# Kernel tuning notes

Measured on AMD Instinct MI355X. Metric: run time of the kernel, lower is better.

The kernel has to match this reference:

```python
import jax, jax.numpy as jnp
import numpy as np

B, T, C, H = 4, 4096, 1024, 64  # batch, seq_len, embedding_dimension, head_size


def setup_inputs() -> dict:
    key = jax.random.key(0)
    kx, kq, kk, kv = jax.random.split(key, 4)
    x = jax.random.normal(kx, (B, T, C), dtype=jnp.float32)
    # nn.Linear(C, H, bias=False) -> weight applied as x @ W with W:[C,H]
    s = 1.0 / np.sqrt(C)
    Wq = jax.random.normal(kq, (C, H), dtype=jnp.float32) * s
    Wk = jax.random.normal(kk, (C, H), dtype=jnp.float32) * s
    Wv = jax.random.normal(kv, (C, H), dtype=jnp.float32) * s
    return {"x": x, "Wq": Wq, "Wk": Wk, "Wv": Wv}


def reference(x, Wq, Wk, Wv):
    Bx, Tx, Cx = x.shape
    q = x @ Wq  # [B,T,H]
    k = x @ Wk  # [B,T,H]
    v = x @ Wv  # [B,T,H]
    # NOTE: original scales by C**-0.5 (embedding dim), not head_size**-0.5
    wei = jnp.einsum('bqh,bkh->bqk', q, k) * (Cx ** -0.5)  # [B,T,T]
    causal = jnp.tril(jnp.ones((Tx, Tx), dtype=bool))
    wei = jnp.where(causal, wei, -jnp.inf)
    wei = jax.nn.softmax(wei, axis=-1)
    out = jnp.einsum('bqk,bkh->bqh', wei, v)  # [B,T,H]
    return out
```

## Files before the change

kernel.cpp:

```cpp
#include <hip/hip_runtime.h>
#include <math.h>

#define BATCH 4
#define SEQ   4096
#define EMB   1024
#define HDIM  64
#define NSPLIT 4

typedef __attribute__((ext_vector_type(8))) short bf16x8;
typedef __attribute__((ext_vector_type(4))) float f32x4;
typedef __attribute__((ext_vector_type(4))) unsigned int u32x4;

#define MFMA16(a, b, c) __builtin_amdgcn_mfma_f32_16x16x32_bf16(a, b, c, 0, 0, 0)

__device__ __forceinline__ unsigned short f2bf(float f) {
  unsigned int u = __float_as_uint(f);
  u = (u + 0x7FFFu + ((u >> 16) & 1u)) >> 16;
  return (unsigned short)u;
}

__device__ __forceinline__ float fexp2(float x) {
  float r;
  asm("v_exp_f32 %0, %1" : "=v"(r) : "v"(x));
  return r;
}

__global__ __launch_bounds__(256) void wt_kernel(
    const float* __restrict__ Wq, const float* __restrict__ Wk,
    const float* __restrict__ Wv, unsigned short* __restrict__ wt) {
  __shared__ float tile[64][65];
  const int bid = blockIdx.x;
  const int m = bid >> 4, kt = bid & 15;
  const float* W = (m == 0) ? Wq : (m == 1) ? Wk : Wv;
  const int tid = threadIdx.x;
  {
    const int r = tid >> 2, c4 = tid & 3;
    const float* src = W + (size_t)(kt * 64 + r) * 64 + c4 * 16;
#pragma unroll
    for (int j = 0; j < 4; ++j) {
      float4 a = *(const float4*)(src + j * 4);
      tile[r][c4 * 16 + j * 4 + 0] = a.x;
      tile[r][c4 * 16 + j * 4 + 1] = a.y;
      tile[r][c4 * 16 + j * 4 + 2] = a.z;
      tile[r][c4 * 16 + j * 4 + 3] = a.w;
    }
  }
  __syncthreads();
  {
    const int col = tid >> 2, kq = tid & 3;
    unsigned short o[16];
#pragma unroll
    for (int j = 0; j < 16; ++j) o[j] = f2bf(tile[kq * 16 + j][col]);
    unsigned short* dst = wt + (size_t)(m * 64 + col) * 1024 + kt * 64 + kq * 16;
    *(bf16x8*)(dst)     = *(bf16x8*)&o[0];
    *(bf16x8*)(dst + 8) = *(bf16x8*)&o[8];
  }
}

__global__ __launch_bounds__(512) void qkv_mfma_kernel(
    const float* __restrict__ x, const unsigned short* __restrict__ wt,
    unsigned short* __restrict__ qb, unsigned short* __restrict__ kb,
    unsigned short* __restrict__ vt) {
  __shared__ __align__(16) unsigned short xs[64 * 64];
  __shared__ __align__(16) unsigned short ws[192 * 64];
  const int tid  = threadIdx.x;
  const int lane = tid & 63, wid = tid >> 6;
  const int g = lane >> 4, p = lane & 15;
  const int mt = wid >> 2, wq = wid & 3;
  const size_t row0 = (size_t)blockIdx.x * 64;

  const int sr = tid >> 3, sc = tid & 7;
  const float* xp = x + (row0 + sr) * EMB + sc * 8;

  f32x4 acc[2][3];
#pragma unroll
  for (int rt = 0; rt < 2; ++rt)
#pragma unroll
    for (int ct = 0; ct < 3; ++ct) acc[rt][ct] = (f32x4){0.f, 0.f, 0.f, 0.f};

  float4 rx[2];
  bf16x8 rw[3];
#pragma unroll
  for (int j = 0; j < 2; ++j) rx[j] = *(const float4*)(xp + j * 4);
#pragma unroll
  for (int it = 0; it < 3; ++it) {
    int i = tid + it * 512, col = i >> 3, cc = i & 7;
    rw[it] = *(const bf16x8*)(wt + (size_t)col * 1024 + cc * 8);
  }

  for (int kc = 0; kc < 16; ++kc) {
    __syncthreads();
#pragma unroll
    for (int j = 0; j < 2; ++j) {
      ushort4 h;
      h.x = f2bf(rx[j].x); h.y = f2bf(rx[j].y);
      h.z = f2bf(rx[j].z); h.w = f2bf(rx[j].w);
      *(ushort4*)((char*)xs + ((sr * 128 + sc * 16 + j * 8) ^ ((sr & 7) << 4))) = h;
    }
#pragma unroll
    for (int it = 0; it < 3; ++it) {
      int i = tid + it * 512, col = i >> 3, cc = i & 7;
      *(bf16x8*)((char*)ws + ((col * 128 + cc * 16) ^ ((col & 7) << 4))) = rw[it];
    }
    if (kc < 15) {
      const float* xpn = xp + (kc + 1) * 64;
#pragma unroll
      for (int j = 0; j < 2; ++j) rx[j] = *(const float4*)(xpn + j * 4);
#pragma unroll
      for (int it = 0; it < 3; ++it) {
        int i = tid + it * 512, col = i >> 3, cc = i & 7;
        rw[it] = *(const bf16x8*)(wt + (size_t)col * 1024 + (kc + 1) * 64 + cc * 8);
      }
    }
    __syncthreads();
#pragma unroll
    for (int ks = 0; ks < 2; ++ks) {
      bf16x8 af[2];
#pragma unroll
      for (int rt = 0; rt < 2; ++rt) {
        int row = mt * 32 + rt * 16 + p;
        af[rt] = *(const bf16x8*)((char*)xs +
                 ((row * 128 + ks * 64 + g * 16) ^ ((row & 7) << 4)));
      }
#pragma unroll
      for (int ct = 0; ct < 3; ++ct) {
        int col = wq * 48 + ct * 16 + p;
        bf16x8 bfr = *(const bf16x8*)((char*)ws +
                     ((col * 128 + ks * 64 + g * 16) ^ ((col & 7) << 4)));
#pragma unroll
        for (int rt = 0; rt < 2; ++rt)
          acc[rt][ct] = MFMA16(af[rt], bfr, acc[rt][ct]);
      }
    }
  }

  const int b     = (int)(row0 >> 12);
  const int tbase = (int)(row0 & 4095);
  unsigned short* vtb = vt + (((size_t)b * 64 + (tbase >> 6)) * 64) * 64;
#pragma unroll
  for (int rt = 0; rt < 2; ++rt)
#pragma unroll
    for (int ct = 0; ct < 3; ++ct) {
      const int c0  = wq * 48 + ct * 16;
      const int mtx = c0 >> 6;
      const int col = (c0 & 63) + p;
#pragma unroll
      for (int r = 0; r < 4; ++r) {
        const int row = mt * 32 + rt * 16 + 4 * g + r;
        const float vf = acc[rt][ct][r];
        if (mtx == 0)      qb[(row0 + row) * HDIM + col] = f2bf(vf * 0.0450843714f);
        else if (mtx == 1) kb[(row0 + row) * HDIM + col] = f2bf(vf);
        else               vtb[(size_t)col * 64 + row]   = f2bf(vf);
      }
    }
}

__device__ __forceinline__ void tile_body_lds(
    const unsigned short* __restrict__ sKb, const unsigned short* __restrict__ sVb,
    int qrel, bool diag,
    const bf16x8& qf0, const bf16x8& qf1,
    int p, int g, int cA0, int cA1, int srcA, int srcB, bool hi,
    float& m, float& l, f32x4 (&o)[4]) {
  f32x4 sc4[4];
#pragma unroll
  for (int t = 0; t < 4; ++t) {
    const int row = 16 * t + p;
    bf16x8 a0 = *(const bf16x8*)((const char*)sKb + row * 128 + cA0);
    bf16x8 a1 = *(const bf16x8*)((const char*)sKb + row * 128 + cA1);
    f32x4 a = (f32x4){0.f, 0.f, 0.f, 0.f};
    a = MFMA16(a0, qf0, a);
    a = MFMA16(a1, qf1, a);
    sc4[t] = a;
  }
  if (diag) {
#pragma unroll
    for (int t = 0; t < 4; ++t)
#pragma unroll
      for (int r = 0; r < 4; ++r)
        if (16 * t + 4 * g + r > qrel) sc4[t][r] = -1e30f;
  }
  float tm = -3e38f;
#pragma unroll
  for (int t = 0; t < 4; ++t)
#pragma unroll
    for (int r = 0; r < 4; ++r) tm = fmaxf(tm, sc4[t][r]);
  tm = fmaxf(tm, __shfl_xor(tm, 16));
  tm = fmaxf(tm, __shfl_xor(tm, 32));
  if (__any(tm > m + 11.5f)) {
    float mn = fmaxf(m, tm);
    float c = fexp2(m - mn);
    l *= c;
#pragma unroll
    for (int mi = 0; mi < 4; ++mi) o[mi] *= c;
    m = mn;
  }
  float psum = 0.f;
#pragma unroll
  for (int t = 0; t < 4; ++t)
#pragma unroll
    for (int r = 0; r < 4; ++r) {
      float pv = fexp2(sc4[t][r] - m);
      sc4[t][r] = pv;
      psum += pv;
    }
  l += psum;
  unsigned int pk[4][2];
#pragma unroll
  for (int t = 0; t < 4; ++t) {
    asm("v_cvt_pk_bf16_f32 %0, %1, %2"
        : "=v"(pk[t][0]) : "v"(sc4[t][0]), "v"(sc4[t][1]));
    asm("v_cvt_pk_bf16_f32 %0, %1, %2"
        : "=v"(pk[t][1]) : "v"(sc4[t][2]), "v"(sc4[t][3]));
  }
  u32x4 wb0, wb1;
#pragma unroll
  for (int h2 = 0; h2 < 2; ++h2) {
    const int src = h2 ? srcB : srcA;
    unsigned c0 = (unsigned)__shfl((int)pk[0][0], src);
    unsigned c1 = (unsigned)__shfl((int)pk[1][0], src);
    wb0[2 * h2 + 0] = hi ? c1 : c0;
    unsigned d0 = (unsigned)__shfl((int)pk[0][1], src);
    unsigned d1 = (unsigned)__shfl((int)pk[1][1], src);
    wb0[2 * h2 + 1] = hi ? d1 : d0;
    unsigned e0 = (unsigned)__shfl((int)pk[2][0], src);
    unsigned e1 = (unsigned)__shfl((int)pk[3][0], src);
    wb1[2 * h2 + 0] = hi ? e1 : e0;
    unsigned f0 = (unsigned)__shfl((int)pk[2][1], src);
    unsigned f1 = (unsigned)__shfl((int)pk[3][1], src);
    wb1[2 * h2 + 1] = hi ? f1 : f0;
  }
  bf16x8 b0 = __builtin_bit_cast(bf16x8, wb0);
  bf16x8 b1 = __builtin_bit_cast(bf16x8, wb1);
#pragma unroll
  for (int mi = 0; mi < 4; ++mi) {
    const int rowv = 16 * mi + p;
    bf16x8 va0 = *(const bf16x8*)((const char*)sVb + rowv * 128 + cA0);
    bf16x8 va1 = *(const bf16x8*)((const char*)sVb + rowv * 128 + cA1);
    o[mi] = MFMA16(va0, b0, o[mi]);
    o[mi] = MFMA16(va1, b1, o[mi]);
  }
}

__device__ __forceinline__ void item_map(int g_it, int j, int& kt, bool& isA, bool& diag) {
  if (g_it <= j) { isA = true;  kt = g_it;         diag = (g_it == j); }
  else           { isA = false; kt = g_it - j - 1; diag = (kt == 63 - j); }
}

__global__ __launch_bounds__(256) void attn_partial_kernel(
    const unsigned short* __restrict__ qb, const unsigned short* __restrict__ kbm,
    const unsigned short* __restrict__ vt, float* __restrict__ pw) {
  __shared__ __align__(16) unsigned short sK[2][4096];
  __shared__ __align__(16) unsigned short sV[2][4096];
  const int tid = threadIdx.x;
  const int wid = tid >> 6, lane = tid & 63;
  const int g = lane >> 4, p = lane & 15;
  const int bid = blockIdx.x;
  const int sp = bid & 3, j = (bid >> 2) & 31, b = bid >> 7;
  const int jB = 63 - j;
  const int tq0A = j * 64 + 16 * wid;
  const int tq0B = jB * 64 + 16 * wid;

  const char* kbase = (const char*)(kbm + (size_t)b * SEQ * HDIM);
  const char* vbase = (const char*)(vt  + (size_t)b * SEQ * HDIM);

  const unsigned short* qrowA = qb + ((size_t)b * SEQ + tq0A + p) * HDIM;
  const bf16x8 qfA0 = *(const bf16x8*)(qrowA + 8 * g);
  const bf16x8 qfA1 = *(const bf16x8*)(qrowA + 32 + 8 * g);
  const unsigned short* qrowB = qb + ((size_t)b * SEQ + tq0B + p) * HDIM;
  const bf16x8 qfB0 = *(const bf16x8*)(qrowB + 8 * g);
  const bf16x8 qfB1 = *(const bf16x8*)(qrowB + 32 + 8 * g);

  const int slot0 = tid * 16, slot1 = slot0 + 4096;
  const int r0 = slot0 >> 7, koff0 = r0 * 128 + ((slot0 & 127) ^ ((r0 & 7) << 4));
  const int r1 = slot1 >> 7, koff1 = r1 * 128 + ((slot1 & 127) ^ ((r1 & 7) << 4));

  const int swz = (p & 7) << 4;
  const int cA0 = (16 * g) ^ swz, cA1 = (64 + 16 * g) ^ swz;

  const int srcA = (g & 1) * 32 + p;
  const int srcB = srcA + 16;
  const bool hi = (g >> 1) != 0;

  float mA = -1e30f, lA = 0.f, mB = -1e30f, lB = 0.f;
  f32x4 oA[4], oB[4];
#pragma unroll
  for (int mi = 0; mi < 4; ++mi) {
    oA[mi] = (f32x4){0.f, 0.f, 0.f, 0.f};
    oB[mi] = (f32x4){0.f, 0.f, 0.f, 0.f};
  }

  const int cnt = (65 - sp + NSPLIT - 1) / NSPLIT;

  bf16x8 rk0, rk1, rv0, rv1;
  {
    int kt; bool isA, diag;
    item_map(sp, j, kt, isA, diag);
    const char* kk = kbase + (size_t)kt * 8192;
    const char* vv = vbase + (size_t)kt * 8192;
    rk0 = *(const bf16x8*)(kk + koff0); rk1 = *(const bf16x8*)(kk + koff1);
    rv0 = *(const bf16x8*)(vv + koff0); rv1 = *(const bf16x8*)(vv + koff1);
  }
  *(bf16x8*)((char*)sK[0] + slot0) = rk0;
  *(bf16x8*)((char*)sK[0] + slot1) = rk1;
  *(bf16x8*)((char*)sV[0] + slot0) = rv0;
  *(bf16x8*)((char*)sV[0] + slot1) = rv1;
  if (cnt > 1) {
    int kt; bool isA, diag;
    item_map(sp + NSPLIT, j, kt, isA, diag);
    const char* kk = kbase + (size_t)kt * 8192;
    const char* vv = vbase + (size_t)kt * 8192;
    rk0 = *(const bf16x8*)(kk + koff0); rk1 = *(const bf16x8*)(kk + koff1);
    rv0 = *(const bf16x8*)(vv + koff0); rv1 = *(const bf16x8*)(vv + koff1);
  }
  __syncthreads();

  for (int ii = 0; ii < cnt; ++ii) {
    const int buf = ii & 1;
    if (ii + 1 < cnt) {
      const int nb = buf ^ 1;
      *(bf16x8*)((char*)sK[nb] + slot0) = rk0;
      *(bf16x8*)((char*)sK[nb] + slot1) = rk1;
      *(bf16x8*)((char*)sV[nb] + slot0) = rv0;
      *(bf16x8*)((char*)sV[nb] + slot1) = rv1;
    }
    if (ii + 2 < cnt) {
      int kt; bool isA, diag;
      item_map(sp + (ii + 2) * NSPLIT, j, kt, isA, diag);
      const char* kk = kbase + (size_t)kt * 8192;
      const char* vv = vbase + (size_t)kt * 8192;
      rk0 = *(const bf16x8*)(kk + koff0); rk1 = *(const bf16x8*)(kk + koff1);
      rv0 = *(const bf16x8*)(vv + koff0); rv1 = *(const bf16x8*)(vv + koff1);
    }
    int kt; bool isA, diag;
    item_map(sp + ii * NSPLIT, j, kt, isA, diag);
    if (isA) {
      tile_body_lds(sK[buf], sV[buf], tq0A + p - kt * 64, diag, qfA0, qfA1,
                    p, g, cA0, cA1, srcA, srcB, hi, mA, lA, oA);
    } else {
      tile_body_lds(sK[buf], sV[buf], tq0B + p - kt * 64, diag, qfB0, qfB1,
                    p, g, cA0, cA1, srcA, srcB, hi, mB, lB, oB);
    }
    __syncthreads();
  }

  lA += __shfl_xor(lA, 16); lA += __shfl_xor(lA, 32);
  lB += __shfl_xor(lB, 16); lB += __shfl_xor(lB, 32);

  {
    const int grpA = j * 4 + wid;
    float* pp = pw + ((size_t)(b * 256 + grpA) * NSPLIT + sp) * 1056;
#pragma unroll
    for (int mi = 0; mi < 4; ++mi)
      *(f32x4*)(pp + p * 64 + 16 * mi + 4 * g) = oA[mi];
    if (g == 0) { pp[1024 + p] = mA; pp[1040 + p] = lA; }
  }
  {
    const int grpB = jB * 4 + wid;
    float* pp = pw + ((size_t)(b * 256 + grpB) * NSPLIT + sp) * 1056;
#pragma unroll
    for (int mi = 0; mi < 4; ++mi)
      *(f32x4*)(pp + p * 64 + 16 * mi + 4 * g) = oB[mi];
    if (g == 0) { pp[1024 + p] = mB; pp[1040 + p] = lB; }
  }
}

__global__ __launch_bounds__(256) void attn_merge_kernel(
    const float* __restrict__ pw, float* __restrict__ out) {
  const int bid = blockIdx.x;
  const int b = bid >> 8, grp = bid & 255;
  const int q = threadIdx.x & 15, db = threadIdx.x >> 4;
  const float* pp = pw + (size_t)bid * NSPLIT * 1056;
  float ms[NSPLIT], ls[NSPLIT];
  float mm = -3e38f;
#pragma unroll
  for (int s = 0; s < NSPLIT; ++s) {
    ms[s] = pp[s * 1056 + 1024 + q];
    ls[s] = pp[s * 1056 + 1040 + q];
    mm = fmaxf(mm, ms[s]);
  }
  float L = 0.f, a0 = 0.f, a1 = 0.f, a2 = 0.f, a3 = 0.f;
#pragma unroll
  for (int s = 0; s < NSPLIT; ++s) {
    float sc = fexp2(ms[s] - mm);
    L += ls[s] * sc;
    float4 v = *(const float4*)(pp + s * 1056 + q * 64 + 4 * db);
    a0 += v.x * sc; a1 += v.y * sc; a2 += v.z * sc; a3 += v.w * sc;
  }
  const float inv = 1.f / L;
  float* op = out + ((size_t)b * SEQ + grp * 16 + q) * HDIM + 4 * db;
  op[0] = a0 * inv; op[1] = a1 * inv; op[2] = a2 * inv; op[3] = a3 * inv;
}

extern "C" void kernel_launch(void* const* d_in, const int* in_sizes, int n_in,
                              void* d_out, int out_size, void* d_ws, size_t ws_size,
                              hipStream_t stream) {
  const float* x  = (const float*)d_in[0];
  const float* Wq = (const float*)d_in[1];
  const float* Wk = (const float*)d_in[2];
  const float* Wv = (const float*)d_in[3];
  float* outp = (float*)d_out;

  const size_t rows = (size_t)BATCH * SEQ;
  unsigned short* qbf = (unsigned short*)d_ws;
  unsigned short* kbf = qbf + rows * HDIM;
  unsigned short* vtb = kbf + rows * HDIM;
  unsigned short* wt  = vtb + rows * HDIM;
  float* pw = (float*)(wt + 192 * 1024);

  wt_kernel<<<dim3(48), dim3(256), 0, stream>>>(Wq, Wk, Wv, wt);
  qkv_mfma_kernel<<<dim3((unsigned)(rows / 64)), dim3(512), 0, stream>>>(x, wt, qbf, kbf, vtb);
  attn_partial_kernel<<<dim3(512), dim3(256), 0, stream>>>(qbf, kbf, vtb, pw);
  attn_merge_kernel<<<dim3(1024), dim3(256), 0, stream>>>(pw, outp);
}
```

Before: 59.00 us.

## Enlarge attention query tile to 128 rows with 8 waves per block

Each attention block now handles two 128-row query tiles (paired front/back for causal balance) using 8 waves instead of 4, so every K/V tile staged in LDS is reused by twice as many waves. Each thread now loads one 16-byte chunk of K and one of V per tile instead of two each. The grid halves to 256 blocks of 512 threads, and the last two key tiles of each query tile take the masked diagonal path. The aim is to halve global and LDS K/V traffic per unit of work. In exchange there is some wasted masked compute on the diagonal tiles, and each block is larger, which changes occupancy.

```diff
diff --git a/kernel.cpp b/kernel.cpp
--- a/kernel.cpp
+++ b/kernel.cpp
@@ -241,12 +241,13 @@
   }
 }
 
-__device__ __forceinline__ void item_map(int g_it, int j, int& kt, bool& isA, bool& diag) {
-  if (g_it <= j) { isA = true;  kt = g_it;         diag = (g_it == j); }
-  else           { isA = false; kt = g_it - j - 1; diag = (kt == 63 - j); }
-}
-
-__global__ __launch_bounds__(256) void attn_partial_kernel(
+__device__ __forceinline__ void item_map128(int g_it, int nA, int nB,
+                                            int& kt, bool& isA, bool& diag) {
+  if (g_it < nA) { isA = true;  kt = g_it;      diag = (kt >= nA - 2); }
+  else           { isA = false; kt = g_it - nA; diag = (kt >= nB - 2); }
+}
+
+__global__ __launch_bounds__(512) void attn_partial_kernel(
     const unsigned short* __restrict__ qb, const unsigned short* __restrict__ kbm,
     const unsigned short* __restrict__ vt, float* __restrict__ pw) {
   __shared__ __align__(16) unsigned short sK[2][4096];
@@ -255,10 +256,11 @@
   const int wid = tid >> 6, lane = tid & 63;
   const int g = lane >> 4, p = lane & 15;
   const int bid = blockIdx.x;
-  const int sp = bid & 3, j = (bid >> 2) & 31, b = bid >> 7;
-  const int jB = 63 - j;
-  const int tq0A = j * 64 + 16 * wid;
-  const int tq0B = jB * 64 + 16 * wid;
+  const int sp = bid & 3, j = (bid >> 2) & 15, b = bid >> 6;
+  const int jB = 31 - j;
+  const int nA = 2 * j + 2, nB = 64 - 2 * j;
+  const int tq0A = j * 128 + 16 * wid;
+  const int tq0B = jB * 128 + 16 * wid;
 
   const char* kbase = (const char*)(kbm + (size_t)b * SEQ * HDIM);
   const char* vbase = (const char*)(vt  + (size_t)b * SEQ * HDIM);
@@ -270,9 +272,8 @@
   const bf16x8 qfB0 = *(const bf16x8*)(qrowB + 8 * g);
   const bf16x8 qfB1 = *(const bf16x8*)(qrowB + 32 + 8 * g);
 
-  const int slot0 = tid * 16, slot1 = slot0 + 4096;
-  const int r0 = slot0 >> 7, koff0 = r0 * 128 + ((slot0 & 127) ^ ((r0 & 7) << 4));
-  const int r1 = slot1 >> 7, koff1 = r1 * 128 + ((slot1 & 127) ^ ((r1 & 7) << 4));
+  const int slot = tid * 16;
+  const int r0 = slot >> 7, koff = r0 * 128 + ((slot & 127) ^ ((r0 & 7) << 4));
 
   const int swz = (p & 7) << 4;
   const int cA0 = (16 * g) ^ swz, cA1 = (64 + 16 * g) ^ swz;
@@ -289,28 +290,22 @@
     oB[mi] = (f32x4){0.f, 0.f, 0.f, 0.f};
   }
 
-  const int cnt = (65 - sp + NSPLIT - 1) / NSPLIT;
-
-  bf16x8 rk0, rk1, rv0, rv1;
+  const int cnt = (66 - sp + NSPLIT - 1) / NSPLIT;
+
+  bf16x8 rk0, rv0;
   {
     int kt; bool isA, diag;
-    item_map(sp, j, kt, isA, diag);
-    const char* kk = kbase + (size_t)kt * 8192;
-    const char* vv = vbase + (size_t)kt * 8192;
-    rk0 = *(const bf16x8*)(kk + koff0); rk1 = *(const bf16x8*)(kk + koff1);
-    rv0 = *(const bf16x8*)(vv + koff0); rv1 = *(const bf16x8*)(vv + koff1);
-  }
-  *(bf16x8*)((char*)sK[0] + slot0) = rk0;
-  *(bf16x8*)((char*)sK[0] + slot1) = rk1;
-  *(bf16x8*)((char*)sV[0] + slot0) = rv0;
-  *(bf16x8*)((char*)sV[0] + slot1) = rv1;
+    item_map128(sp, nA, nB, kt, isA, diag);
+    rk0 = *(const bf16x8*)(kbase + (size_t)kt * 8192 + koff);
+    rv0 = *(const bf16x8*)(vbase + (size_t)kt * 8192 + koff);
+  }
+  *(bf16x8*)((char*)sK[0] + slot) = rk0;
+  *(bf16x8*)((char*)sV[0] + slot) = rv0;
   if (cnt > 1) {
     int kt; bool isA, diag;
-    item_map(sp + NSPLIT, j, kt, isA, diag);
-    const char* kk = kbase + (size_t)kt * 8192;
-    const char* vv = vbase + (size_t)kt * 8192;
-    rk0 = *(const bf16x8*)(kk + koff0); rk1 = *(const bf16x8*)(kk + koff1);
-    rv0 = *(const bf16x8*)(vv + koff0); rv1 = *(const bf16x8*)(vv + koff1);
+    item_map128(sp + NSPLIT, nA, nB, kt, isA, diag);
+    rk0 = *(const bf16x8*)(kbase + (size_t)kt * 8192 + koff);
+    rv0 = *(const bf16x8*)(vbase + (size_t)kt * 8192 + koff);
   }
   __syncthreads();
 
@@ -318,21 +313,17 @@
     const int buf = ii & 1;
     if (ii + 1 < cnt) {
       const int nb = buf ^ 1;
-      *(bf16x8*)((char*)sK[nb] + slot0) = rk0;
-      *(bf16x8*)((char*)sK[nb] + slot1) = rk1;
-      *(bf16x8*)((char*)sV[nb] + slot0) = rv0;
-      *(bf16x8*)((char*)sV[nb] + slot1) = rv1;
+      *(bf16x8*)((char*)sK[nb] + slot) = rk0;
+      *(bf16x8*)((char*)sV[nb] + slot) = rv0;
     }
     if (ii + 2 < cnt) {
       int kt; bool isA, diag;
-      item_map(sp + (ii + 2) * NSPLIT, j, kt, isA, diag);
-      const char* kk = kbase + (size_t)kt * 8192;
-      const char* vv = vbase + (size_t)kt * 8192;
-      rk0 = *(const bf16x8*)(kk + koff0); rk1 = *(const bf16x8*)(kk + koff1);
-      rv0 = *(const bf16x8*)(vv + koff0); rv1 = *(const bf16x8*)(vv + koff1);
+      item_map128(sp + (ii + 2) * NSPLIT, nA, nB, kt, isA, diag);
+      rk0 = *(const bf16x8*)(kbase + (size_t)kt * 8192 + koff);
+      rv0 = *(const bf16x8*)(vbase + (size_t)kt * 8192 + koff);
     }
     int kt; bool isA, diag;
-    item_map(sp + ii * NSPLIT, j, kt, isA, diag);
+    item_map128(sp + ii * NSPLIT, nA, nB, kt, isA, diag);
     if (isA) {
       tile_body_lds(sK[buf], sV[buf], tq0A + p - kt * 64, diag, qfA0, qfA1,
                     p, g, cA0, cA1, srcA, srcB, hi, mA, lA, oA);
@@ -347,7 +338,7 @@
   lB += __shfl_xor(lB, 16); lB += __shfl_xor(lB, 32);
 
   {
-    const int grpA = j * 4 + wid;
+    const int grpA = j * 8 + wid;
     float* pp = pw + ((size_t)(b * 256 + grpA) * NSPLIT + sp) * 1056;
 #pragma unroll
     for (int mi = 0; mi < 4; ++mi)
@@ -355,7 +346,7 @@
     if (g == 0) { pp[1024 + p] = mA; pp[1040 + p] = lA; }
   }
   {
-    const int grpB = jB * 4 + wid;
+    const int grpB = jB * 8 + wid;
     float* pp = pw + ((size_t)(b * 256 + grpB) * NSPLIT + sp) * 1056;
 #pragma unroll
     for (int mi = 0; mi < 4; ++mi)
@@ -409,6 +400,6 @@
 
   wt_kernel<<<dim3(48), dim3(256), 0, stream>>>(Wq, Wk, Wv, wt);
   qkv_mfma_kernel<<<dim3((unsigned)(rows / 64)), dim3(512), 0, stream>>>(x, wt, qbf, kbf, vtb);
-  attn_partial_kernel<<<dim3(512), dim3(256), 0, stream>>>(qbf, kbf, vtb, pw);
+  attn_partial_kernel<<<dim3(256), dim3(512), 0, stream>>>(qbf, kbf, vtb, pw);
   attn_merge_kernel<<<dim3(1024), dim3(256), 0, stream>>>(pw, outp);
 }
```

Measured after the change: 58.00 us. About the same (-1.7%).
